# Optimization experiments

Measured on AMD Instinct MI355X. Metric: run time of the kernel, lower is better.

## Reference

```python
import jax, jax.numpy as jnp
import numpy as np

AX = (-2, -1)
LAMBDA = 0.05
ITERS = 6

# torch fft_2d_img  = fftshift(ifft2(ifftshift(x)))  (used in the FORWARD model)
# torch ifft_2d_img = ifftshift(fft2(fftshift(x)))   (used in the ADJOINT model)

def _fwd_xform(x):
    return jnp.fft.fftshift(jnp.fft.ifft2(jnp.fft.ifftshift(x, axes=AX), axes=AX, norm='ortho'), axes=AX)

def _adj_xform(x):
    return jnp.fft.ifftshift(jnp.fft.fft2(jnp.fft.fftshift(x, axes=AX), axes=AX, norm='ortho'), axes=AX)

def _forward_model(img, S, mask):
    # img [b,t,h,w] -> masked multicoil k-space [b,t,c,h,w]
    return mask * _fwd_xform(S * img[:, :, None])

def _adjoint_model(k, S):
    # k [b,t,c,h,w] -> coil-combined image [b,t,h,w]
    return jnp.sum(jnp.conj(S) * _adj_xform(k), axis=2)

def _system_matrix_R(p, S, L, mask):
    # p [b,sv,h,w]; L [b,t,sv]
    expanded = jnp.einsum('bts,bshw->bthw', L, p)
    combined = _adjoint_model(_forward_model(expanded, S, mask), S)
    out = jnp.einsum('bts,bthw->bshw', jnp.conj(L), combined)
    return out + LAMBDA * p

def _cg_solve(b_vec, S, L, mask):
    z0 = jnp.zeros_like(b_vec)
    rs0 = jnp.vdot(b_vec, b_vec)

    def step(carry, _):
        z, r, p, rs_old, done = carry
        Ap = _system_matrix_R(p, S, L, mask)
        alpha = rs_old / (jnp.vdot(p, Ap) + 1e-20)
        z_n = z + alpha * p
        r_n = r - alpha * Ap
        rs_new = jnp.vdot(r_n, r_n)
        p_n = r_n + (rs_new / (rs_old + 1e-20)) * p
        # replicate torch early-break: freeze state once residual is tiny
        z_o = jnp.where(done, z, z_n)
        r_o = jnp.where(done, r, r_n)
        p_o = jnp.where(done, p, p_n)
        rs_o = jnp.where(done, rs_old, rs_new)
        done_n = done | (jnp.abs(rs_o) < 1e-10)
        return (z_o, r_o, p_o, rs_o, done_n), None

    carry0 = (z0, b_vec, b_vec, rs0, jnp.array(False))
    (z, _, _, _, _), _ = jax.lax.scan(step, carry0, None, length=ITERS)
    return z

def setup_inputs() -> dict:
    key = jax.random.key(0)
    ks = jax.random.split(key, 9)
    b, t, c, h, w, sv = 2, 12, 10, 256, 256, 3
    f32 = jnp.float32
    inp = {
        'k_real': jax.random.normal(ks[0], (b, t, c, h, w), f32),
        'k_imag': jax.random.normal(ks[1], (b, t, c, h, w), f32),
        'mo_real': jax.random.normal(ks[2], (b, sv, h, w), f32),
        'mo_imag': jax.random.normal(ks[3], (b, sv, h, w), f32),
        's_real': jax.random.normal(ks[4], (b, 1, c, h, w), f32),
        's_imag': jax.random.normal(ks[5], (b, 1, c, h, w), f32),
        'tb_real': jax.random.normal(ks[6], (b, t, sv), f32),
        'tb_imag': jax.random.normal(ks[7], (b, t, sv), f32),
        'mask': (jax.random.uniform(ks[8], (b, t, 1, h, w)) < 0.35).astype(f32),
    }
    return inp

def reference(k_real, k_imag, mo_real, mo_imag, s_real, s_imag, tb_real, tb_imag, mask):
    Y = k_real + 1j * k_imag          # [b,t,c,h,w]
    MO = mo_real + 1j * mo_imag       # [b,sv,h,w]
    S = s_real + 1j * s_imag          # [b,1,c,h,w]
    L = tb_real + 1j * tb_imag        # [b,t,sv]
    # b = L^H A^H Y + lambda * model_output
    b_vec = jnp.einsum('bts,bthw->bshw', jnp.conj(L), _adjoint_model(Y, S)) + LAMBDA * MO
    z = _cg_solve(b_vec, S, L, mask)  # [b,sv,h,w] complex
    return jnp.stack([z.real, z.imag], axis=-1)  # [b,sv,h,w,2] float32
```

## Files before the change

kernel.cpp:

```cpp
#include <hip/hip_runtime.h>
#include <math.h>

#define HW 65536
#define LAM 0.05f

struct Scal {
  double pap_re, pap_im, rq_re, rq_im, qq;
  double rs_old, al_re, al_im, beta;
  int done, apply, cnt, pad;
};

__device__ __forceinline__ float2 cadd(float2 a, float2 b){ return make_float2(a.x+b.x, a.y+b.y); }
__device__ __forceinline__ float2 csub(float2 a, float2 b){ return make_float2(a.x-b.x, a.y-b.y); }
__device__ __forceinline__ float2 cmul(float2 a, float2 b){
  return make_float2(a.x*b.x - a.y*b.y, a.x*b.y + a.y*b.x);
}
__device__ __forceinline__ float2 cmulj(float2 a, float2 b){
  return make_float2(a.x*b.x + a.y*b.y, a.x*b.y - a.y*b.x);
}
__device__ __forceinline__ int swz(int p){ return p ^ (p>>4); }

__device__ __forceinline__ void wave_lds_sync(){
  __builtin_amdgcn_wave_barrier();
  __asm__ __volatile__("s_waitcnt lgkmcnt(0)" ::: "memory");
  __builtin_amdgcn_wave_barrier();
}

template<int S>
__device__ __forceinline__ void bfly4(float2 x0, float2 x1, float2 x2, float2 x3,
                                      float2& y0, float2& y1, float2& y2, float2& y3){
  float2 a  = cadd(x0,x2), bm = csub(x0,x2);
  float2 c  = cadd(x1,x3), d  = csub(x1,x3);
  float2 jd = make_float2(-(float)S*d.y, (float)S*d.x);
  y0 = cadd(a,c); y2 = csub(a,c); y1 = cadd(bm,jd); y3 = csub(bm,jd);
}

template<int S>
__device__ __forceinline__ void dft16(float2* a){
  const float s_ = (float)S;
  const float2 W1 = make_float2( 0.92387953251f,  s_*0.38268343236f);
  const float2 W2 = make_float2( 0.70710678119f,  s_*0.70710678119f);
  const float2 W3 = make_float2( 0.38268343236f,  s_*0.92387953251f);
  const float2 W4_ = make_float2(0.f,              s_*1.f);
  const float2 W6 = make_float2(-0.70710678119f,  s_*0.70710678119f);
  const float2 W9 = make_float2(-0.92387953251f, -s_*0.38268343236f);
  float2 t[16];
#pragma unroll
  for (int n0=0;n0<4;n0++){
    float2 y0,y1,y2,y3;
    bfly4<S>(a[n0], a[n0+4], a[n0+8], a[n0+12], y0,y1,y2,y3);
    if (n0==1){ y1=cmul(y1,W1); y2=cmul(y2,W2); y3=cmul(y3,W3); }
    if (n0==2){ y1=cmul(y1,W2); y2=cmul(y2,W4_); y3=cmul(y3,W6); }
    if (n0==3){ y1=cmul(y1,W3); y2=cmul(y2,W6); y3=cmul(y3,W9); }
    t[n0*4+0]=y0; t[n0*4+1]=y1; t[n0*4+2]=y2; t[n0*4+3]=y3;
  }
#pragma unroll
  for (int k1=0;k1<4;k1++){
    float2 y0,y1,y2,y3;
    bfly4<S>(t[0*4+k1], t[1*4+k1], t[2*4+k1], t[3*4+k1], y0,y1,y2,y3);
    a[k1+0]=y0; a[k1+4]=y1; a[k1+8]=y2; a[k1+12]=y3;
  }
}

template<int S>
__device__ void fft256_r16(float2* buf, int l){
  float2 a[16];
#pragma unroll
  for (int j=0;j<16;j++) a[j] = buf[swz(l + 16*j)];
  dft16<S>(a);
  float ang = (float)S * 6.2831853071795865f * (float)l * (1.f/256.f);
  float sn, cs; __sincosf(ang, &sn, &cs);
  float2 wstep = make_float2(cs, sn);
  float2 w = wstep;
#pragma unroll
  for (int k=1;k<16;k++){ a[k] = cmul(a[k], w); w = cmul(w, wstep); }
#pragma unroll
  for (int k=0;k<16;k++) buf[swz(16*k + l)] = a[k];
  wave_lds_sync();
#pragma unroll
  for (int j=0;j<16;j++) a[j] = buf[swz(16*l + j)];
  dft16<S>(a);
  wave_lds_sync();
#pragma unroll
  for (int k=0;k<16;k++) buf[swz(l + 16*k)] = a[k];
  wave_lds_sync();
}

__global__ __launch_bounds__(256) void k_w(const float* __restrict__ mask,
                                           const float* __restrict__ tbr,
                                           const float* __restrict__ tbi,
                                           float* __restrict__ Wf,
                                           Scal* sc){
  if (blockIdx.x==0 && blockIdx.y==0 && threadIdx.x==0){
    sc->pap_re=0.0; sc->pap_im=0.0; sc->rq_re=0.0; sc->rq_im=0.0; sc->qq=0.0;
    sc->rs_old=0.0; sc->al_re=0.0; sc->al_im=0.0; sc->beta=0.0;
    sc->done=0; sc->apply=0; sc->cnt=0;
  }
  __shared__ float wtf[9][16][17];
  int tid = threadIdx.x;
  int bx = blockIdx.x;
  int b  = blockIdx.y;
  int u0 = (bx>>4)<<4, v0 = (bx&15)<<4;
  int u_l = tid>>4, v_l = tid&15;
  int pix = (u0+u_l)*256 + (v0+v_l);
  float d0=0,d1=0,d2=0, o01r=0,o01i=0, o02r=0,o02i=0, o12r=0,o12i=0;
#pragma unroll
  for (int t=0;t<12;t++){
    float m = mask[(size_t)(b*12+t)*HW + pix];
    int lb = (b*12+t)*3;
    float l0r = tbr[lb+0], l0i = tbi[lb+0];
    float l1r = tbr[lb+1], l1i = tbi[lb+1];
    float l2r = tbr[lb+2], l2i = tbi[lb+2];
    d0 += m*(l0r*l0r + l0i*l0i);
    d1 += m*(l1r*l1r + l1i*l1i);
    d2 += m*(l2r*l2r + l2i*l2i);
    o01r += m*(l0r*l1r + l0i*l1i); o01i += m*(l0r*l1i - l0i*l1r);
    o02r += m*(l0r*l2r + l0i*l2i); o02i += m*(l0r*l2i - l0i*l2r);
    o12r += m*(l1r*l2r + l1i*l2i); o12i += m*(l1r*l2i - l1i*l2r);
  }
  const float s = 1.0f/65536.0f;
  wtf[0][u_l][v_l] = d0*s;   wtf[1][u_l][v_l] = d1*s;   wtf[2][u_l][v_l] = d2*s;
  wtf[3][u_l][v_l] = o01r*s; wtf[4][u_l][v_l] = o01i*s;
  wtf[5][u_l][v_l] = o02r*s; wtf[6][u_l][v_l] = o02i*s;
  wtf[7][u_l][v_l] = o12r*s; wtf[8][u_l][v_l] = o12i*s;
  __syncthreads();
  int u_l2 = tid&15, v_l2 = tid>>4;
  float* W0 = Wf + (size_t)b*9*HW;
  float4* WA = (float4*)W0;
  float4* WB = (float4*)(W0 + (size_t)4*HW);
  float*  WC = W0 + (size_t)8*HW;
  size_t wb = (size_t)(v0+v_l2)*256 + (u0+u_l2);
  WA[wb] = make_float4(wtf[0][u_l2][v_l2], wtf[1][u_l2][v_l2],
                       wtf[2][u_l2][v_l2], wtf[3][u_l2][v_l2]);
  WB[wb] = make_float4(wtf[4][u_l2][v_l2], wtf[5][u_l2][v_l2],
                       wtf[6][u_l2][v_l2], wtf[7][u_l2][v_l2]);
  WC[wb] = wtf[8][u_l2][v_l2];
}

__global__ __launch_bounds__(640) void k_yrow(const float* __restrict__ kr,
                                              const float* __restrict__ ki,
                                              const float* __restrict__ tbr,
                                              const float* __restrict__ tbi,
                                              float2* __restrict__ bufA){
  __shared__ float2 lb[30*257];
  int tid = threadIdx.x;
  int r = blockIdx.x, b = blockIdx.y;
  {
    int c = tid>>6, px4 = tid&63;
    float ar[3][4], ai[3][4];
#pragma unroll
    for (int s=0;s<3;s++)
#pragma unroll
      for (int j=0;j<4;j++){ ar[s][j]=0.f; ai[s][j]=0.f; }
#pragma unroll
    for (int t=0;t<12;t++){
      size_t off = ((size_t)((b*12+t)*10+c))*HW + (size_t)r*256 + 4*px4;
      float4 yr4 = *(const float4*)(kr + off);
      float4 yi4 = *(const float4*)(ki + off);
      int lbi = (b*12+t)*3;
      float l0r = tbr[lbi+0], l0i = tbi[lbi+0];
      float l1r = tbr[lbi+1], l1i = tbi[lbi+1];
      float l2r = tbr[lbi+2], l2i = tbi[lbi+2];
      float yrj[4] = {yr4.x, yr4.y, yr4.z, yr4.w};
      float yij[4] = {yi4.x, yi4.y, yi4.z, yi4.w};
#pragma unroll
      for (int j=0;j<4;j++){
        float yr = yrj[j], yi = yij[j];
        ar[0][j] += l0r*yr + l0i*yi;  ai[0][j] += l0r*yi - l0i*yr;
        ar[1][j] += l1r*yr + l1i*yi;  ai[1][j] += l1r*yi - l1i*yr;
        ar[2][j] += l2r*yr + l2i*yi;  ai[2][j] += l2r*yi - l2i*yr;
      }
    }
#pragma unroll
    for (int j=0;j<4;j++){
      int px = 4*px4 + j;
      float sg = (((r ^ px) & 1) ? -1.f : 1.f) * (1.f/256.f);
      int sk = swz(px);
#pragma unroll
      for (int s=0;s<3;s++)
        lb[(c*3+s)*257 + sk] = make_float2(ar[s][j]*sg, ai[s][j]*sg);
    }
  }
  __syncthreads();
  int wv = tid>>6, lane = tid&63, g = lane>>4, l = lane&15;
  int tau = 4*wv + g;
  if (tau < 30){
    float2* lw = &lb[tau*257];
    fft256_r16<-1>(lw, l);
    float2* dst = bufA + (size_t)(b*30+tau)*HW + (size_t)r*256;
#pragma unroll
    for (int j=0;j<8;j++){
      int e = 2*(16*j + l);
      float2 e0 = lw[swz(e)], e1 = lw[swz(e+1)];
      *(float4*)(dst + e) = make_float4(e0.x,e0.y,e1.x,e1.y);
    }
  }
}

template<int MODE>
__global__ __launch_bounds__(384) void k_colpass(float2* __restrict__ bufA,
                                                 const float* __restrict__ Wf){
  __shared__ float2 lb[24*257];
  int tid = threadIdx.x;
  int wv = tid>>6, lane = tid&63, g = lane>>4, l = lane&15;
  int j0 = blockIdx.x*8;
  int c = blockIdx.y, b = blockIdx.z;
#pragma unroll
  for (int it=0; it<8; it++){
    int idx = it*384 + tid;
    int s = idx>>10, rem = idx&1023, u = rem>>2, cp = rem&3;
    const float2* src = bufA + (size_t)(b*30 + c*3 + s)*HW;
    float4 v = *(const float4*)(src + u*256 + j0 + 2*cp);
    lb[(s*8+2*cp  )*257 + swz(u)] = make_float2(v.x, v.y);
    lb[(s*8+2*cp+1)*257 + swz(u)] = make_float2(v.z, v.w);
  }
  __syncthreads();
  int tau = 4*wv + g;
  if (MODE==0){
    fft256_r16<-1>(&lb[tau*257], l);
  } else {
    fft256_r16<1>(&lb[tau*257], l);
    __syncthreads();
    const float* W0 = Wf + (size_t)b*9*HW;
    const float4* WA = (const float4*)W0;
    const float4* WB = (const float4*)(W0 + (size_t)4*HW);
    const float*  WC = W0 + (size_t)8*HW;
    for (int idx=tid; idx<2048; idx+=384){
      int u = idx&255, col = idx>>8;
      int su = swz(u);
      int v = j0 + col;
      float2 x0 = lb[(0*8+col)*257 + su];
      float2 x1 = lb[(1*8+col)*257 + su];
      float2 x2 = lb[(2*8+col)*257 + su];
      size_t wb = (size_t)v*256 + u;
      float4 wa = WA[wb];
      float4 wbv = WB[wb];
      float d0 = wa.x, d1 = wa.y, d2 = wa.z, o01r = wa.w;
      float o01i = wbv.x, o02r = wbv.y, o02i = wbv.z, o12r = wbv.w;
      float o12i = WC[wb];
      float2 y0, y1, y2;
      y0.x = d0*x0.x + o01r*x1.x - o01i*x1.y + o02r*x2.x - o02i*x2.y;
      y0.y = d0*x0.y + o01r*x1.y + o01i*x1.x + o02r*x2.y + o02i*x2.x;
      y1.x = o01r*x0.x + o01i*x0.y + d1*x1.x + o12r*x2.x - o12i*x2.y;
      y1.y = o01r*x0.y - o01i*x0.x + d1*x1.y + o12r*x2.y + o12i*x2.x;
      y2.x = o02r*x0.x + o02i*x0.y + o12r*x1.x + o12i*x1.y + d2*x2.x;
      y2.y = o02r*x0.y - o02i*x0.x + o12r*x1.y - o12i*x1.x + d2*x2.y;
      lb[(0*8+col)*257 + su] = y0;
      lb[(1*8+col)*257 + su] = y1;
      lb[(2*8+col)*257 + su] = y2;
    }
    __syncthreads();
    fft256_r16<-1>(&lb[tau*257], l);
  }
  __syncthreads();
#pragma unroll
  for (int it=0; it<8; it++){
    int idx = it*384 + tid;
    int s = idx>>10, rem = idx&1023, u = rem>>2, cp = rem&3;
    float2* dst = bufA + (size_t)(b*30 + c*3 + s)*HW;
    float2 e0 = lb[(s*8+2*cp  )*257 + swz(u)];
    float2 e1 = lb[(s*8+2*cp+1)*257 + swz(u)];
    *(float4*)(dst + u*256 + j0 + 2*cp) = make_float4(e0.x, e0.y, e1.x, e1.y);
  }
}

__global__ __launch_bounds__(512) void k_bsp(const float* __restrict__ sr_,
                                             const float* __restrict__ si_,
                                             const float* __restrict__ mor,
                                             const float* __restrict__ moi,
                                             float2* __restrict__ z,
                                             float2* __restrict__ rvec,
                                             float2* __restrict__ p,
                                             float2* __restrict__ bufA,
                                             Scal* sc){
  __shared__ float2 lb[30*257];
  __shared__ float2 pb[3][256];
  __shared__ double sd[8];
  int tid = threadIdx.x;
  int wv = tid>>6, lane = tid&63, g = lane>>4, l = lane&15;
  int r = blockIdx.x, b = blockIdx.y;
  int px = tid & 255, h = tid >> 8, sk = swz(px);
  float2 sv5[5];
#pragma unroll
  for (int k=0;k<5;k++){
    int c = h + 2*k;
    size_t so = (size_t)(b*10+c)*HW + (size_t)r*256 + px;
    sv5[k] = make_float2(sr_[so], si_[so]);
  }
  float mo_r[3], mo_i[3];
  if (h==0){
#pragma unroll
    for (int s=0;s<3;s++){
      size_t oi = (size_t)(b*3+s)*HW + (size_t)r*256 + px;
      mo_r[s] = mor[oi]; mo_i[s] = moi[oi];
    }
  }
  int tau = 4*wv + g;
  if (tau < 30){
    const float2* src = bufA + (size_t)(b*30+tau)*HW + (size_t)r*256;
    float2* lw = &lb[tau*257];
#pragma unroll
    for (int j=0;j<8;j++){
      int e = 2*(16*j + l);
      float4 v = *(const float4*)(src + e);
      lw[swz(e)]   = make_float2(v.x, v.y);
      lw[swz(e+1)] = make_float2(v.z, v.w);
    }
  }
  __syncthreads();
  float2 a0={0,0}, a1={0,0}, a2={0,0};
#pragma unroll
  for (int k=0;k<5;k++){
    a0 = cadd(a0, cmulj(sv5[k], lb[((h+2*k)*3+0)*257 + sk]));
    a1 = cadd(a1, cmulj(sv5[k], lb[((h+2*k)*3+1)*257 + sk]));
    a2 = cadd(a2, cmulj(sv5[k], lb[((h+2*k)*3+2)*257 + sk]));
  }
  if (h==1){ pb[0][px]=a0; pb[1][px]=a1; pb[2][px]=a2; }
  __syncthreads();
  double dre = 0.0;
  if (h==0){
    a0 = cadd(a0, pb[0][px]);
    a1 = cadd(a1, pb[1][px]);
    a2 = cadd(a2, pb[2][px]);
    float sgl = (((r ^ px) & 1) ? -1.f : 1.f) * LAM;
    a0.x += sgl*mo_r[0]; a0.y += sgl*mo_i[0];
    a1.x += sgl*mo_r[1]; a1.y += sgl*mo_i[1];
    a2.x += sgl*mo_r[2]; a2.y += sgl*mo_i[2];
    float2 accs[3] = {a0,a1,a2};
#pragma unroll
    for (int s=0;s<3;s++){
      size_t oi = (size_t)(b*3+s)*HW + (size_t)r*256 + px;
      z[oi] = make_float2(0.f,0.f);
      rvec[oi] = accs[s]; p[oi] = accs[s];
      dre += (double)accs[s].x*accs[s].x + (double)accs[s].y*accs[s].y;
    }
    pb[0][px]=a0; pb[1][px]=a1; pb[2][px]=a2;
  }
  for (int off=32; off>0; off>>=1) dre += __shfl_down(dre, off, 64);
  if (lane==0) sd[wv] = dre;
  __syncthreads();
  if (tid==0){
    double t=0;
#pragma unroll
    for (int q=0;q<8;q++) t += sd[q];
    atomicAdd(&sc->rs_old, t);
  }
  {
    float2 pv0 = pb[0][px], pv1 = pb[1][px], pv2 = pb[2][px];
#pragma unroll
    for (int k=0;k<5;k++){
      int c = h + 2*k;
      lb[(c*3+0)*257 + sk] = cmul(sv5[k], pv0);
      lb[(c*3+1)*257 + sk] = cmul(sv5[k], pv1);
      lb[(c*3+2)*257 + sk] = cmul(sv5[k], pv2);
    }
  }
  __syncthreads();
  if (tau < 30){
    float2* lw = &lb[tau*257];
    fft256_r16<1>(lw, l);
    float2* dst = bufA + (size_t)(b*30+tau)*HW + (size_t)r*256;
#pragma unroll
    for (int j=0;j<8;j++){
      int e = 2*(16*j + l);
      float2 e0 = lw[swz(e)], e1 = lw[swz(e+1)];
      *(float4*)(dst + e) = make_float4(e0.x,e0.y,e1.x,e1.y);
    }
  }
}

__global__ __launch_bounds__(512) void k_spfft(float2* __restrict__ p,
                                               float2* __restrict__ rvec,
                                               float2* __restrict__ z,
                                               const float2* __restrict__ Ap,
                                               const float* __restrict__ sr_,
                                               const float* __restrict__ si_,
                                               float2* __restrict__ bufA,
                                               Scal* sc){
  __shared__ float2 lb[30*257];
  __shared__ float2 pbuf[3][256];
  int tid = threadIdx.x;
  int wv = tid>>6, lane = tid&63, g = lane>>4, l = lane&15;
  int r = blockIdx.x, b = blockIdx.y;
  int px = tid & 255, h = tid >> 8, sk = swz(px);
  float2 sv5[5];
#pragma unroll
  for (int k=0;k<5;k++){
    int c = h + 2*k;
    size_t so = (size_t)(b*10+c)*HW + (size_t)r*256 + px;
    sv5[k] = make_float2(sr_[so], si_[so]);
  }
  int ap = sc->apply;
  float2 alpha = make_float2((float)sc->al_re, (float)sc->al_im);
  float beta = (float)sc->beta;
  for (int i = tid; i < 768; i += 512){
    int s = i>>8, ppx = i&255;
    size_t oi = (size_t)(b*3+s)*HW + (size_t)r*256 + ppx;
    float2 pvv = p[oi];
    if (ap){
      float2 zv = z[oi], rv = rvec[oi], apv = Ap[oi];
      zv = cadd(zv, cmul(alpha, pvv));
      rv = csub(rv, cmul(alpha, apv));
      float2 pn = make_float2(rv.x + beta*pvv.x, rv.y + beta*pvv.y);
      z[oi] = zv; rvec[oi] = rv; p[oi] = pn;
      pvv = pn;
    }
    pbuf[s][ppx] = pvv;
  }
  __syncthreads();
  {
    float2 pv0 = pbuf[0][px], pv1 = pbuf[1][px], pv2 = pbuf[2][px];
#pragma unroll
    for (int k=0;k<5;k++){
      int c = h + 2*k;
      lb[(c*3+0)*257 + sk] = cmul(sv5[k], pv0);
      lb[(c*3+1)*257 + sk] = cmul(sv5[k], pv1);
      lb[(c*3+2)*257 + sk] = cmul(sv5[k], pv2);
    }
  }
  __syncthreads();
  int tau = 4*wv + g;
  if (tau < 30){
    float2* lw = &lb[tau*257];
    fft256_r16<1>(lw, l);
    float2* dst = bufA + (size_t)(b*30+tau)*HW + (size_t)r*256;
#pragma unroll
    for (int j=0;j<8;j++){
      int e = 2*(16*j + l);
      float2 e0 = lw[swz(e)], e1 = lw[swz(e+1)];
      *(float4*)(dst + e) = make_float4(e0.x,e0.y,e1.x,e1.y);
    }
  }
}

__global__ __launch_bounds__(512) void k_rowcomb(const float2* __restrict__ bufA,
                                                 const float* __restrict__ sr_,
                                                 const float* __restrict__ si_,
                                                 const float2* __restrict__ pvec,
                                                 const float2* __restrict__ rvec,
                                                 float2* __restrict__ Ap,
                                                 Scal* sc){
  __shared__ float2 lb[30*257];
  __shared__ float2 part[3][256];
  __shared__ double sd[5][4];
  int tid = threadIdx.x;
  int wv = tid>>6, lane = tid&63, g = lane>>4, l = lane&15;
  int r = blockIdx.x, b = blockIdx.y;
  int px = tid & 255, h = tid >> 8, sk = swz(px);
  float2 sv5[5];
#pragma unroll
  for (int k=0;k<5;k++){
    int c = h + 2*k;
    size_t so = (size_t)(b*10+c)*HW + (size_t)r*256 + px;
    sv5[k] = make_float2(sr_[so], si_[so]);
  }
  float2 av3[3], rv3[3];
  if (h==0){
#pragma unroll
    for (int s=0;s<3;s++){
      size_t oi = (size_t)(b*3+s)*HW + (size_t)r*256 + px;
      av3[s] = pvec[oi]; rv3[s] = rvec[oi];
    }
  }
  int tau = 4*wv + g;
  if (tau < 30){
    const float2* src = bufA + (size_t)(b*30+tau)*HW + (size_t)r*256;
    float2* lw = &lb[tau*257];
#pragma unroll
    for (int j=0;j<8;j++){
      int e = 2*(16*j + l);
      float4 v = *(const float4*)(src + e);
      lw[swz(e)]   = make_float2(v.x, v.y);
      lw[swz(e+1)] = make_float2(v.z, v.w);
    }
    wave_lds_sync();
    fft256_r16<-1>(lw, l);
  }
  __syncthreads();
  float2 a0={0,0}, a1={0,0}, a2={0,0};
#pragma unroll
  for (int k=0;k<5;k++){
    a0 = cadd(a0, cmulj(sv5[k], lb[((h+2*k)*3+0)*257 + sk]));
    a1 = cadd(a1, cmulj(sv5[k], lb[((h+2*k)*3+1)*257 + sk]));
    a2 = cadd(a2, cmulj(sv5[k], lb[((h+2*k)*3+2)*257 + sk]));
  }
  if (h==1){ part[0][px]=a0; part[1][px]=a1; part[2][px]=a2; }
  __syncthreads();
  double d0=0.0, d1=0.0, d2=0.0, d3=0.0, d4=0.0;
  if (tid < 256){
    a0 = cadd(a0, part[0][px]);
    a1 = cadd(a1, part[1][px]);
    a2 = cadd(a2, part[2][px]);
    float2 accs[3] = {a0,a1,a2};
#pragma unroll
    for (int s=0;s<3;s++){
      size_t oi = (size_t)(b*3+s)*HW + (size_t)r*256 + px;
      float2 acc = accs[s];
      float2 av = av3[s];
      float2 rv = rv3[s];
      acc.x += LAM*av.x; acc.y += LAM*av.y;
      Ap[oi] = acc;
      d0 += (double)av.x*acc.x + (double)av.y*acc.y;
      d1 += (double)av.x*acc.y - (double)av.y*acc.x;
      d2 += (double)rv.x*acc.x + (double)rv.y*acc.y;
      d3 += (double)rv.x*acc.y - (double)rv.y*acc.x;
      d4 += (double)acc.x*acc.x + (double)acc.y*acc.y;
    }
  }
  for (int off=32; off>0; off>>=1){
    d0 += __shfl_down(d0, off, 64);
    d1 += __shfl_down(d1, off, 64);
    d2 += __shfl_down(d2, off, 64);
    d3 += __shfl_down(d3, off, 64);
    d4 += __shfl_down(d4, off, 64);
  }
  if (lane==0 && wv<4){ sd[0][wv]=d0; sd[1][wv]=d1; sd[2][wv]=d2; sd[3][wv]=d3; sd[4][wv]=d4; }
  __syncthreads();
  if (tid==0){
    double t0=0,t1=0,t2=0,t3=0,t4=0;
#pragma unroll
    for (int q=0;q<4;q++){ t0+=sd[0][q]; t1+=sd[1][q]; t2+=sd[2][q]; t3+=sd[3][q]; t4+=sd[4][q]; }
    atomicAdd(&sc->pap_re, t0); atomicAdd(&sc->pap_im, t1);
    atomicAdd(&sc->rq_re,  t2); atomicAdd(&sc->rq_im,  t3);
    atomicAdd(&sc->qq,     t4);
    int total = (int)(gridDim.x*gridDim.y);
    int prev = atomicAdd(&sc->cnt, 1);
    if (prev == total-1){
      sc->cnt = 0;
      if (!sc->done){
        double pr = sc->pap_re + 1e-20, pi = sc->pap_im;
        double den = pr*pr + pi*pi;
        double rs = sc->rs_old;
        double alr =  rs*pr/den, ali = -rs*pi/den;
        double rs_new = rs - 2.0*(alr*sc->rq_re - ali*sc->rq_im)
                           + (alr*alr + ali*ali)*sc->qq;
        sc->al_re = alr; sc->al_im = ali;
        sc->beta = rs_new/(rs + 1e-20);
        sc->rs_old = rs_new;
        sc->apply = 1;
        if (fabs(rs_new) < 1e-10) sc->done = 1;
      } else {
        sc->apply = 0;
      }
      sc->pap_re=0.0; sc->pap_im=0.0; sc->rq_re=0.0; sc->rq_im=0.0; sc->qq=0.0;
    }
  }
}

__global__ __launch_bounds__(256) void k_out(const float2* __restrict__ z,
                                             const float2* __restrict__ p,
                                             const Scal* sc,
                                             float* __restrict__ out){
  int i = blockIdx.x*256 + threadIdx.x;
  int pix = i & (HW-1);
  float sgn = (((pix>>8)^pix)&1) ? -1.f : 1.f;
  float2 zv = z[i];
  if (sc->apply){
    float2 alpha = make_float2((float)sc->al_re, (float)sc->al_im);
    zv = cadd(zv, cmul(alpha, p[i]));
  }
  out[2*i]   = sgn*zv.x;
  out[2*i+1] = sgn*zv.y;
}

extern "C" void kernel_launch(void* const* d_in, const int* in_sizes, int n_in,
                              void* d_out, int out_size, void* d_ws, size_t ws_size,
                              hipStream_t stream){
  const float* kr   = (const float*)d_in[0];
  const float* ki   = (const float*)d_in[1];
  const float* mor  = (const float*)d_in[2];
  const float* moi  = (const float*)d_in[3];
  const float* sr   = (const float*)d_in[4];
  const float* si   = (const float*)d_in[5];
  const float* tbr  = (const float*)d_in[6];
  const float* tbi  = (const float*)d_in[7];
  const float* mask = (const float*)d_in[8];
  float* out = (float*)d_out;

  float2* ws   = (float2*)d_ws;
  float2* bufA = ws;
  float*  Wf   = (float*)(ws + 3932160);
  float2* z    = ws + 4521984;
  float2* r    = ws + 4915200;
  float2* p    = ws + 5308416;
  float2* Ap   = ws + 5701632;
  Scal*   sc   = (Scal*)(ws + 6094848);

  k_w<<<dim3(256,2),dim3(256),0,stream>>>(mask, tbr, tbi, Wf, sc);
  k_yrow<<<dim3(256,2),dim3(640),0,stream>>>(kr, ki, tbr, tbi, bufA);
  k_colpass<0><<<dim3(32,10,2),dim3(384),0,stream>>>(bufA, Wf);
  k_bsp<<<dim3(256,2),dim3(512),0,stream>>>(sr, si, mor, moi, z, r, p,
                                            bufA, sc);
  for (int it=0; it<6; ++it){
    if (it > 0)
      k_spfft<<<dim3(256,2),dim3(512),0,stream>>>(p, r, z, Ap, sr, si, bufA, sc);
    k_colpass<1><<<dim3(32,10,2),dim3(384),0,stream>>>(bufA, Wf);
    k_rowcomb<<<dim3(256,2),dim3(512),0,stream>>>(bufA, sr, si, p, r, Ap, sc);
  }
  k_out<<<dim3(1536),dim3(256),0,stream>>>(z, p, sc, out);
}
```

Baseline: 719.7 us.

## Split row FFT kernels across spatial-vector index for smaller, more numerous blocks

The per-iteration row-FFT kernels (spread and combine) now launch one block per (row, sv, batch) with 192 threads, where before one 512-thread block handled all three sv components. Each block works on 10 coil FFTs instead of 30, so it needs less LDS and the grid holds three times as many blocks, which should raise occupancy and parallelism. In exchange, the coil sensitivity maps are read three times as often (once per sv), and twice as many blocks do atomic reductions into the scalar struct.

```diff
diff --git a/kernel.cpp b/kernel.cpp
--- a/kernel.cpp
+++ b/kernel.cpp
@@ -369,33 +369,24 @@
   }
 }
 
-__global__ __launch_bounds__(512) void k_spfft(float2* __restrict__ p,
-                                               float2* __restrict__ rvec,
-                                               float2* __restrict__ z,
-                                               const float2* __restrict__ Ap,
-                                               const float* __restrict__ sr_,
-                                               const float* __restrict__ si_,
-                                               float2* __restrict__ bufA,
-                                               Scal* sc){
-  __shared__ float2 lb[30*257];
-  __shared__ float2 pbuf[3][256];
+__global__ __launch_bounds__(192) void k_spfft_s(float2* __restrict__ p,
+                                                 float2* __restrict__ rvec,
+                                                 float2* __restrict__ z,
+                                                 const float2* __restrict__ Ap,
+                                                 const float* __restrict__ sr_,
+                                                 const float* __restrict__ si_,
+                                                 float2* __restrict__ bufA,
+                                                 Scal* sc){
+  __shared__ float2 lb[10*257];
+  __shared__ float2 pbuf[256];
   int tid = threadIdx.x;
   int wv = tid>>6, lane = tid&63, g = lane>>4, l = lane&15;
-  int r = blockIdx.x, b = blockIdx.y;
-  int px = tid & 255, h = tid >> 8, sk = swz(px);
-  float2 sv5[5];
-#pragma unroll
-  for (int k=0;k<5;k++){
-    int c = h + 2*k;
-    size_t so = (size_t)(b*10+c)*HW + (size_t)r*256 + px;
-    sv5[k] = make_float2(sr_[so], si_[so]);
-  }
+  int r = blockIdx.x, s = blockIdx.y, b = blockIdx.z;
   int ap = sc->apply;
   float2 alpha = make_float2((float)sc->al_re, (float)sc->al_im);
   float beta = (float)sc->beta;
-  for (int i = tid; i < 768; i += 512){
-    int s = i>>8, ppx = i&255;
-    size_t oi = (size_t)(b*3+s)*HW + (size_t)r*256 + ppx;
+  for (int i = tid; i < 256; i += 192){
+    size_t oi = (size_t)(b*3+s)*HW + (size_t)r*256 + i;
     float2 pvv = p[oi];
     if (ap){
       float2 zv = z[oi], rv = rvec[oi], apv = Ap[oi];
@@ -405,25 +396,28 @@
       z[oi] = zv; rvec[oi] = rv; p[oi] = pn;
       pvv = pn;
     }
-    pbuf[s][ppx] = pvv;
-  }
-  __syncthreads();
-  {
-    float2 pv0 = pbuf[0][px], pv1 = pbuf[1][px], pv2 = pbuf[2][px];
-#pragma unroll
-    for (int k=0;k<5;k++){
-      int c = h + 2*k;
-      lb[(c*3+0)*257 + sk] = cmul(sv5[k], pv0);
-      lb[(c*3+1)*257 + sk] = cmul(sv5[k], pv1);
-      lb[(c*3+2)*257 + sk] = cmul(sv5[k], pv2);
-    }
-  }
-  __syncthreads();
-  int tau = 4*wv + g;
-  if (tau < 30){
-    float2* lw = &lb[tau*257];
+    pbuf[i] = pvv;
+  }
+  __syncthreads();
+  for (int idx = tid; idx < 640; idx += 192){
+    int c = idx>>6, px4 = idx&63;
+    size_t so = (size_t)(b*10+c)*HW + (size_t)r*256 + 4*px4;
+    float4 s4r = *(const float4*)(sr_ + so);
+    float4 s4i = *(const float4*)(si_ + so);
+    float srj[4] = {s4r.x, s4r.y, s4r.z, s4r.w};
+    float sij[4] = {s4i.x, s4i.y, s4i.z, s4i.w};
+#pragma unroll
+    for (int j=0;j<4;j++){
+      int px = 4*px4 + j;
+      lb[c*257 + swz(px)] = cmul(make_float2(srj[j], sij[j]), pbuf[px]);
+    }
+  }
+  __syncthreads();
+  int slot = 4*wv + g;
+  if (slot < 10){
+    float2* lw = &lb[slot*257];
     fft256_r16<1>(lw, l);
-    float2* dst = bufA + (size_t)(b*30+tau)*HW + (size_t)r*256;
+    float2* dst = bufA + (size_t)(b*30 + slot*3 + s)*HW + (size_t)r*256;
 #pragma unroll
     for (int j=0;j<8;j++){
       int e = 2*(16*j + l);
@@ -433,39 +427,22 @@
   }
 }
 
-__global__ __launch_bounds__(512) void k_rowcomb(const float2* __restrict__ bufA,
-                                                 const float* __restrict__ sr_,
-                                                 const float* __restrict__ si_,
-                                                 const float2* __restrict__ pvec,
-                                                 const float2* __restrict__ rvec,
-                                                 float2* __restrict__ Ap,
-                                                 Scal* sc){
-  __shared__ float2 lb[30*257];
-  __shared__ float2 part[3][256];
-  __shared__ double sd[5][4];
+__global__ __launch_bounds__(192) void k_rowcomb_s(const float2* __restrict__ bufA,
+                                                   const float* __restrict__ sr_,
+                                                   const float* __restrict__ si_,
+                                                   const float2* __restrict__ pvec,
+                                                   const float2* __restrict__ rvec,
+                                                   float2* __restrict__ Ap,
+                                                   Scal* sc){
+  __shared__ float2 lb[10*257];
+  __shared__ double sd[5][3];
   int tid = threadIdx.x;
   int wv = tid>>6, lane = tid&63, g = lane>>4, l = lane&15;
-  int r = blockIdx.x, b = blockIdx.y;
-  int px = tid & 255, h = tid >> 8, sk = swz(px);
-  float2 sv5[5];
-#pragma unroll
-  for (int k=0;k<5;k++){
-    int c = h + 2*k;
-    size_t so = (size_t)(b*10+c)*HW + (size_t)r*256 + px;
-    sv5[k] = make_float2(sr_[so], si_[so]);
-  }
-  float2 av3[3], rv3[3];
-  if (h==0){
-#pragma unroll
-    for (int s=0;s<3;s++){
-      size_t oi = (size_t)(b*3+s)*HW + (size_t)r*256 + px;
-      av3[s] = pvec[oi]; rv3[s] = rvec[oi];
-    }
-  }
-  int tau = 4*wv + g;
-  if (tau < 30){
-    const float2* src = bufA + (size_t)(b*30+tau)*HW + (size_t)r*256;
-    float2* lw = &lb[tau*257];
+  int r = blockIdx.x, s = blockIdx.y, b = blockIdx.z;
+  int slot = 4*wv + g;
+  if (slot < 10){
+    const float2* src = bufA + (size_t)(b*30 + slot*3 + s)*HW + (size_t)r*256;
+    float2* lw = &lb[slot*257];
 #pragma unroll
     for (int j=0;j<8;j++){
       int e = 2*(16*j + l);
@@ -477,35 +454,26 @@
     fft256_r16<-1>(lw, l);
   }
   __syncthreads();
-  float2 a0={0,0}, a1={0,0}, a2={0,0};
-#pragma unroll
-  for (int k=0;k<5;k++){
-    a0 = cadd(a0, cmulj(sv5[k], lb[((h+2*k)*3+0)*257 + sk]));
-    a1 = cadd(a1, cmulj(sv5[k], lb[((h+2*k)*3+1)*257 + sk]));
-    a2 = cadd(a2, cmulj(sv5[k], lb[((h+2*k)*3+2)*257 + sk]));
-  }
-  if (h==1){ part[0][px]=a0; part[1][px]=a1; part[2][px]=a2; }
-  __syncthreads();
   double d0=0.0, d1=0.0, d2=0.0, d3=0.0, d4=0.0;
-  if (tid < 256){
-    a0 = cadd(a0, part[0][px]);
-    a1 = cadd(a1, part[1][px]);
-    a2 = cadd(a2, part[2][px]);
-    float2 accs[3] = {a0,a1,a2};
-#pragma unroll
-    for (int s=0;s<3;s++){
-      size_t oi = (size_t)(b*3+s)*HW + (size_t)r*256 + px;
-      float2 acc = accs[s];
-      float2 av = av3[s];
-      float2 rv = rv3[s];
-      acc.x += LAM*av.x; acc.y += LAM*av.y;
-      Ap[oi] = acc;
-      d0 += (double)av.x*acc.x + (double)av.y*acc.y;
-      d1 += (double)av.x*acc.y - (double)av.y*acc.x;
-      d2 += (double)rv.x*acc.x + (double)rv.y*acc.y;
-      d3 += (double)rv.x*acc.y - (double)rv.y*acc.x;
-      d4 += (double)acc.x*acc.x + (double)acc.y*acc.y;
-    }
+  for (int i = tid; i < 256; i += 192){
+    size_t oi = (size_t)(b*3+s)*HW + (size_t)r*256 + i;
+    float2 av = pvec[oi];
+    float2 rv = rvec[oi];
+    int sk = swz(i);
+    float2 acc = make_float2(0.f, 0.f);
+#pragma unroll
+    for (int c=0;c<10;c++){
+      size_t so = (size_t)(b*10+c)*HW + (size_t)r*256 + i;
+      float2 sv = make_float2(sr_[so], si_[so]);
+      acc = cadd(acc, cmulj(sv, lb[c*257 + sk]));
+    }
+    acc.x += LAM*av.x; acc.y += LAM*av.y;
+    Ap[oi] = acc;
+    d0 += (double)av.x*acc.x + (double)av.y*acc.y;
+    d1 += (double)av.x*acc.y - (double)av.y*acc.x;
+    d2 += (double)rv.x*acc.x + (double)rv.y*acc.y;
+    d3 += (double)rv.x*acc.y - (double)rv.y*acc.x;
+    d4 += (double)acc.x*acc.x + (double)acc.y*acc.y;
   }
   for (int off=32; off>0; off>>=1){
     d0 += __shfl_down(d0, off, 64);
@@ -514,16 +482,16 @@
     d3 += __shfl_down(d3, off, 64);
     d4 += __shfl_down(d4, off, 64);
   }
-  if (lane==0 && wv<4){ sd[0][wv]=d0; sd[1][wv]=d1; sd[2][wv]=d2; sd[3][wv]=d3; sd[4][wv]=d4; }
+  if (lane==0){ sd[0][wv]=d0; sd[1][wv]=d1; sd[2][wv]=d2; sd[3][wv]=d3; sd[4][wv]=d4; }
   __syncthreads();
   if (tid==0){
     double t0=0,t1=0,t2=0,t3=0,t4=0;
 #pragma unroll
-    for (int q=0;q<4;q++){ t0+=sd[0][q]; t1+=sd[1][q]; t2+=sd[2][q]; t3+=sd[3][q]; t4+=sd[4][q]; }
+    for (int q=0;q<3;q++){ t0+=sd[0][q]; t1+=sd[1][q]; t2+=sd[2][q]; t3+=sd[3][q]; t4+=sd[4][q]; }
     atomicAdd(&sc->pap_re, t0); atomicAdd(&sc->pap_im, t1);
     atomicAdd(&sc->rq_re,  t2); atomicAdd(&sc->rq_im,  t3);
     atomicAdd(&sc->qq,     t4);
-    int total = (int)(gridDim.x*gridDim.y);
+    int total = (int)(gridDim.x*gridDim.y*gridDim.z);
     int prev = atomicAdd(&sc->cnt, 1);
     if (prev == total-1){
       sc->cnt = 0;
@@ -593,9 +561,11 @@
                                             bufA, sc);
   for (int it=0; it<6; ++it){
     if (it > 0)
-      k_spfft<<<dim3(256,2),dim3(512),0,stream>>>(p, r, z, Ap, sr, si, bufA, sc);
+      k_spfft_s<<<dim3(256,3,2),dim3(192),0,stream>>>(p, r, z, Ap, sr, si,
+                                                      bufA, sc);
     k_colpass<1><<<dim3(32,10,2),dim3(384),0,stream>>>(bufA, Wf);
-    k_rowcomb<<<dim3(256,2),dim3(512),0,stream>>>(bufA, sr, si, p, r, Ap, sc);
+    k_rowcomb_s<<<dim3(256,3,2),dim3(192),0,stream>>>(bufA, sr, si, p, r,
+                                                      Ap, sc);
   }
   k_out<<<dim3(1536),dim3(256),0,stream>>>(z, p, sc, out);
 }
```

Result: slower. 1.083 ms (+50.4%).

## Split spfft kernel per subspace component into smaller 192-thread blocks

Applied to the files above, without the earlier changes.

The row-FFT kernel now launches one block per (row, subspace component, batch) with 192 threads and a 10-row LDS buffer, in place of one 512-thread block handling all 30 coil×component rows. This cuts LDS per block and triples the grid, so more blocks can be resident and the load is spread more evenly across CUs. Coil sensitivities are now read with float4 vector loads. The cost is that each sensitivity row is loaded three times, once per component block, and the CG update is spread across blocks by component.

```diff
diff --git a/kernel.cpp b/kernel.cpp
--- a/kernel.cpp
+++ b/kernel.cpp
@@ -369,33 +369,24 @@
   }
 }
 
-__global__ __launch_bounds__(512) void k_spfft(float2* __restrict__ p,
-                                               float2* __restrict__ rvec,
-                                               float2* __restrict__ z,
-                                               const float2* __restrict__ Ap,
-                                               const float* __restrict__ sr_,
-                                               const float* __restrict__ si_,
-                                               float2* __restrict__ bufA,
-                                               Scal* sc){
-  __shared__ float2 lb[30*257];
-  __shared__ float2 pbuf[3][256];
+__global__ __launch_bounds__(192) void k_spfft_s(float2* __restrict__ p,
+                                                 float2* __restrict__ rvec,
+                                                 float2* __restrict__ z,
+                                                 const float2* __restrict__ Ap,
+                                                 const float* __restrict__ sr_,
+                                                 const float* __restrict__ si_,
+                                                 float2* __restrict__ bufA,
+                                                 Scal* sc){
+  __shared__ float2 lb[10*257];
+  __shared__ float2 pbuf[256];
   int tid = threadIdx.x;
   int wv = tid>>6, lane = tid&63, g = lane>>4, l = lane&15;
-  int r = blockIdx.x, b = blockIdx.y;
-  int px = tid & 255, h = tid >> 8, sk = swz(px);
-  float2 sv5[5];
-#pragma unroll
-  for (int k=0;k<5;k++){
-    int c = h + 2*k;
-    size_t so = (size_t)(b*10+c)*HW + (size_t)r*256 + px;
-    sv5[k] = make_float2(sr_[so], si_[so]);
-  }
+  int r = blockIdx.x, s = blockIdx.y, b = blockIdx.z;
   int ap = sc->apply;
   float2 alpha = make_float2((float)sc->al_re, (float)sc->al_im);
   float beta = (float)sc->beta;
-  for (int i = tid; i < 768; i += 512){
-    int s = i>>8, ppx = i&255;
-    size_t oi = (size_t)(b*3+s)*HW + (size_t)r*256 + ppx;
+  for (int i = tid; i < 256; i += 192){
+    size_t oi = (size_t)(b*3+s)*HW + (size_t)r*256 + i;
     float2 pvv = p[oi];
     if (ap){
       float2 zv = z[oi], rv = rvec[oi], apv = Ap[oi];
@@ -405,25 +396,28 @@
       z[oi] = zv; rvec[oi] = rv; p[oi] = pn;
       pvv = pn;
     }
-    pbuf[s][ppx] = pvv;
-  }
-  __syncthreads();
-  {
-    float2 pv0 = pbuf[0][px], pv1 = pbuf[1][px], pv2 = pbuf[2][px];
-#pragma unroll
-    for (int k=0;k<5;k++){
-      int c = h + 2*k;
-      lb[(c*3+0)*257 + sk] = cmul(sv5[k], pv0);
-      lb[(c*3+1)*257 + sk] = cmul(sv5[k], pv1);
-      lb[(c*3+2)*257 + sk] = cmul(sv5[k], pv2);
-    }
-  }
-  __syncthreads();
-  int tau = 4*wv + g;
-  if (tau < 30){
-    float2* lw = &lb[tau*257];
+    pbuf[i] = pvv;
+  }
+  __syncthreads();
+  for (int idx = tid; idx < 640; idx += 192){
+    int c = idx>>6, px4 = idx&63;
+    size_t so = (size_t)(b*10+c)*HW + (size_t)r*256 + 4*px4;
+    float4 s4r = *(const float4*)(sr_ + so);
+    float4 s4i = *(const float4*)(si_ + so);
+    float srj[4] = {s4r.x, s4r.y, s4r.z, s4r.w};
+    float sij[4] = {s4i.x, s4i.y, s4i.z, s4i.w};
+#pragma unroll
+    for (int j=0;j<4;j++){
+      int px = 4*px4 + j;
+      lb[c*257 + swz(px)] = cmul(make_float2(srj[j], sij[j]), pbuf[px]);
+    }
+  }
+  __syncthreads();
+  int slot = 4*wv + g;
+  if (slot < 10){
+    float2* lw = &lb[slot*257];
     fft256_r16<1>(lw, l);
-    float2* dst = bufA + (size_t)(b*30+tau)*HW + (size_t)r*256;
+    float2* dst = bufA + (size_t)(b*30 + slot*3 + s)*HW + (size_t)r*256;
 #pragma unroll
     for (int j=0;j<8;j++){
       int e = 2*(16*j + l);
@@ -593,7 +587,8 @@
                                             bufA, sc);
   for (int it=0; it<6; ++it){
     if (it > 0)
-      k_spfft<<<dim3(256,2),dim3(512),0,stream>>>(p, r, z, Ap, sr, si, bufA, sc);
+      k_spfft_s<<<dim3(256,3,2),dim3(192),0,stream>>>(p, r, z, Ap, sr, si,
+                                                      bufA, sc);
     k_colpass<1><<<dim3(32,10,2),dim3(384),0,stream>>>(bufA, Wf);
     k_rowcomb<<<dim3(256,2),dim3(512),0,stream>>>(bufA, sr, si, p, r, Ap, sc);
   }
```

New measurement: 736.4 us. 2.3% more time.
